# Optimization experiments

Measured on AMD Instinct MI355X. Metric: run time of the kernel, lower is better.

## Reference

```python
import jax, jax.numpy as jnp
import numpy as np


def setup_inputs() -> dict:
    key = jax.random.key(0)
    ks = jax.random.split(key, 32)
    B, S, H, E, Vs, T = 32, 400, 512, 300, 200, 32
    EN, V = 50000, 50200
    rn = lambda k, shape, s=0.05: jax.random.normal(k, shape, jnp.float32) * s
    return {
        'encoder_hidden': rn(ks[0], (B, S, 2 * H), 1.0),
        'hidden0': rn(ks[1], (B, H), 1.0),
        'user_embed': rn(ks[2], (B, E), 1.0),
        'W_embed': rn(ks[3], (EN, E), 1.0),
        'W_ih': rn(ks[4], (3 * H, E)), 'W_hh': rn(ks[5], (3 * H, H)),
        'b_ih': rn(ks[6], (3 * H,)), 'b_hh': rn(ks[7], (3 * H,)),
        'Wk_c': rn(ks[8], (2 * H, H)), 'bk_c': rn(ks[9], (H,)),
        'Wq_c': rn(ks[10], (H, H)), 'bq_c': rn(ks[11], (H,)),
        'we_c': rn(ks[12], (H,)), 'be_c': rn(ks[13], (1,)),
        'Wk_u': rn(ks[14], (E, H)), 'bk_u': rn(ks[15], (H,)),
        'Wq_u': rn(ks[16], (H, H)), 'bq_u': rn(ks[17], (H,)),
        'we_u': rn(ks[18], (H,)), 'be_u': rn(ks[19], (1,)),
        'Wc': rn(ks[20], (3 * H + 2 * E, H)),
        'Wg': rn(ks[21], (3 * H + E,)), 'bg': rn(ks[22], (1,)),
        'Wgen': rn(ks[23], (H, EN)),
        'src_mask': jnp.ones((B, S), jnp.int32),
        'tgt_': jax.random.randint(ks[24], (B, T), 0, EN),
        'specific_vocab': jax.random.randint(ks[25], (B, Vs), 0, EN),
        'vocab_size': V,
    }


def reference(encoder_hidden, hidden0, user_embed, W_embed, W_ih, W_hh, b_ih, b_hh,
              Wk_c, bk_c, Wq_c, bq_c, we_c, be_c, Wk_u, bk_u, Wq_u, bq_u, we_u, be_u,
              Wc, Wg, bg, Wgen, src_mask, tgt_, specific_vocab, vocab_size):
    B, T = tgt_.shape
    # teacher forcing: prev token embed, step 0 uses <s> token id 1
    tgt_embed = W_embed[tgt_]                                  # [B,T,E]
    init_embed = jnp.broadcast_to(W_embed[1], (B, 1, W_embed.shape[1]))
    prev = jnp.concatenate([init_embed, tgt_embed[:, :T - 1]], axis=1)
    xs = jnp.swapaxes(prev, 0, 1)                              # [T,B,E]

    user_vocab_emb = W_embed[specific_vocab]                   # [B,Vs,E]
    proj_key_c = encoder_hidden @ Wk_c + bk_c                  # [B,S,H]
    proj_key_u = user_vocab_emb @ Wk_u + bk_u                  # [B,Vs,H]
    mask = src_mask != 0
    batch_idx = jnp.arange(B)[:, None]

    def gru_cell(h, x):
        gi = x @ W_ih.T + b_ih
        gh = h @ W_hh.T + b_hh
        i_r, i_z, i_n = jnp.split(gi, 3, axis=-1)
        h_r, h_z, h_n = jnp.split(gh, 3, axis=-1)
        r = jax.nn.sigmoid(i_r + h_r)
        z = jax.nn.sigmoid(i_z + h_z)
        n = jnp.tanh(i_n + r * h_n)
        return (1.0 - z) * n + z * h

    def step(h, x):
        h = gru_cell(h, x)                                     # [B,H]
        q = h
        # Bahdanau attention over encoder states
        sc = jnp.tanh((q @ Wq_c + bq_c)[:, None, :] + proj_key_c) @ we_c + be_c  # [B,S]
        sc = jnp.where(mask, sc, -1e9)
        ac = jax.nn.softmax(sc, axis=-1)
        ctx_c = jnp.einsum('bs,bsd->bd', ac, encoder_hidden)   # [B,2H]
        # Bahdanau attention over user-specific vocab embeddings
        su = jnp.tanh((q @ Wq_u + bq_u)[:, None, :] + proj_key_u) @ we_u + be_u  # [B,Vs]
        au = jax.nn.softmax(su, axis=-1)
        ctx_u = jnp.einsum('bv,bve->be', au, user_vocab_emb)   # [B,E]
        ch = jnp.tanh(jnp.concatenate([q, ctx_c, ctx_u, user_embed], axis=-1) @ Wc)
        gen_prob = jax.nn.softmax(ch @ Wgen, axis=-1)          # [B,embed_num]
        gen_prob = jnp.pad(gen_prob, ((0, 0), (0, vocab_size - gen_prob.shape[-1])))
        copy_prob = jnp.zeros((B, vocab_size), gen_prob.dtype).at[batch_idx, specific_vocab].add(au)
        copy_p = jax.nn.sigmoid(jnp.concatenate([ctx_c, q, ctx_u], axis=-1) @ Wg + bg[0])[:, None]
        mix = copy_p * copy_prob + (1.0 - copy_p) * gen_prob   # [B,vocab]
        return h, mix

    _, probs = jax.lax.scan(step, hidden0, xs)                 # [T,B,V]
    return jnp.swapaxes(probs, 0, 1)                           # [B,T,V]
```

## Files before the change

kernel.cpp:

```cpp
#include <hip/hip_runtime.h>


typedef __attribute__((ext_vector_type(8))) short short8;
typedef __attribute__((ext_vector_type(4))) float f32x4;
typedef unsigned short us;

#define SCW (-2.8853900817779268f)

__device__ __forceinline__ float bf2f(us u) {
  return __uint_as_float(((unsigned)u) << 16);
}
__device__ __forceinline__ us f2bf(float f) {
  unsigned x = __float_as_uint(f);
  unsigned r = x + 0x7fffu + ((x >> 16) & 1u);
  return (us)(r >> 16);
}
__device__ __forceinline__ float fsigmoid(float x) { return 1.f / (1.f + __expf(-x)); }
__device__ __forceinline__ float ftanh(float x) {
  float t = __expf(-2.f * fabsf(x));
  float r = (1.f - t) / (1.f + t);
  return x >= 0.f ? r : -r;
}
__device__ __forceinline__ float ftanh_fast(float x) {
  float u = exp2f(SCW * fabsf(x));
  float r = (1.f - u) * __builtin_amdgcn_rcpf(1.f + u);
  return copysignf(r, x);
}

struct PP {
  const float *enc, *hidden0, *Wk_c, *Wk_u, *Wq_c, *Wq_u, *Wc, *W_ih, *W_hh, *W_embed;
  const int *tgt, *sv;
  us *encb, *hball, *WkcT, *WkuT, *WqcuT, *WcT, *WihT, *WhhF, *xe, *uve;
};

__device__ void tcast_job(const float* __restrict__ src, us* __restrict__ dst,
                          int R, int C, int Rpad, int x, int y, float scale,
                          int lt, float* tb) {
  int tx = lt & 31, ty = lt >> 5;
  int c0 = x * 32, r0 = y * 32;
#pragma unroll
  for (int i = 0; i < 4; ++i) {
// ... 252 lines not shown
#pragma unroll
    for (int q = 0; q < 2; ++q)
#pragma unroll
      for (int reg = 0; reg < 4; ++reg) {
        int r = m0 + m * 16 + (lane >> 4) * 4 + reg;
        int c = n0 + (w * 2 + q) * 16 + (lane & 15);
        float v = acc[m][q][reg];
        if (MODE == 0) v += bscale * bias[c];
        else v = ftanh_fast(v);
        outB[(size_t)r * N + c] = f2bf(v);
      }
}

struct FP {
  const us* frag; const us* gib; const float* bhh; const float* hidden0;
  us* hball; float* hfall; int* arrive;
  const us* xe; const us* WihT; const float* bih; us* gibout;
  const us* encb; const us* WkcT; const float* bkc; us* pkc;
  const us* uve; const us* WkuT; const float* bku; us* pku;
  const float* Wgen; us* WT;
  const float* enc; us* encTp;
  us* uveTp;
};

__device__ void gru_body(const FP& P, int q, int tid, char* pool) {
  us* hs = (us*)pool;
  float* gh = (float*)(pool + 32768);
  const int lane = tid & 63, w = tid >> 6;
  short8 bfr[16];
  {
    const us* fb = P.frag + (((size_t)(q * 12 + w) * 16) * 64 + lane) * 8;
#pragma unroll
    for (int kt = 0; kt < 16; ++kt) bfr[kt] = *(const short8*)(fb + (size_t)kt * 512);
  }
  float hprev[3];
#pragma unroll
  for (int s = 0; s < 3; ++s) {
    int i = tid + s * 768;
    if (i < 2048) {
      int b = i >> 6, jj = i & 63;
      hprev[s] = P.hidden0[b * 512 + q * 64 + jj];
    }
  }
  if (tid == 0) {
    while (__hip_atomic_load(P.arrive + 32, __ATOMIC_ACQUIRE,
                             __HIP_MEMORY_SCOPE_AGENT) < 48) {
      __builtin_amdgcn_s_sleep(1);
    }
  }
  __syncthreads();
  const int sw = (lane & 7) << 3;
  for (int t = 0; t < 32; ++t) {
    if (t > 0) {
      if (tid == 0) {
        while (__hip_atomic_load(P.arrive + (t - 1), __ATOMIC_ACQUIRE,
                                 __HIP_MEMORY_SCOPE_AGENT) < 8) {
          __builtin_amdgcn_s_sleep(1);
        }
      }
      __syncthreads();
    }
    const us* hp = P.hball + (size_t)t * 16384;
    for (int i = tid; i < 2048; i += 768)
      ((uint4*)hs)[i ^ ((i >> 6) & 7)] = *(const uint4*)(hp + i * 8);
    __syncthreads();
    f32x4 acc0 = {}, acc1 = {};
#pragma unroll
// ... 3 lines not shown
      short8 a0 = *(const short8*)(hs + base0);
      short8 a1 = *(const short8*)(hs + base1);
      acc0 = __builtin_amdgcn_mfma_f32_16x16x32_bf16(a0, bfr[kt], acc0, 0, 0, 0);
      acc1 = __builtin_amdgcn_mfma_f32_16x16x32_bf16(a1, bfr[kt], acc1, 0, 0, 0);
    }
    {
      int col = w * 16 + (lane & 15);
#pragma unroll
      for (int reg = 0; reg < 4; ++reg) {
        gh[col * 33 + ((lane >> 4) * 4 + reg)] = acc0[reg];
        gh[col * 33 + (16 + (lane >> 4) * 4 + reg)] = acc1[reg];
      }
    }
    __syncthreads();
    us* hbn = P.hball + (size_t)(t + 1) * 16384;
    float* hfn = P.hfall + (size_t)t * 16384;
#pragma unroll
    for (int s = 0; s < 3; ++s) {
      int i = tid + s * 768;
      if (i < 2048) {
        int b = i >> 6, jj = i & 63, j = q * 64 + jj;
        float g0 = gh[jj * 33 + b] + P.bhh[j];
        float g1 = gh[(64 + jj) * 33 + b] + P.bhh[512 + j];
        float g2 = gh[(128 + jj) * 33 + b] + P.bhh[1024 + j];
        size_t gbase = (size_t)(t * 32 + b) * 1536;
        float r_ = fsigmoid(bf2f(P.gib[gbase + j]) + g0);
        float z_ = fsigmoid(bf2f(P.gib[gbase + 512 + j]) + g1);
        float n_ = ftanh(bf2f(P.gib[gbase + 1024 + j]) + r_ * g2);
        float hv = (1.f - z_) * n_ + z_ * hprev[s];
        hprev[s] = hv;
        hbn[b * 512 + j] = f2bf(hv);
        hfn[b * 512 + j] = hv;
      }
    }
    __syncthreads();
    if (tid == 0)
      __hip_atomic_fetch_add(P.arrive + t, 1, __ATOMIC_RELEASE,
                             __HIP_MEMORY_SCOPE_AGENT);
  }
}

__device__ void gemm0_body(const us* A, const us* BT, int N, int K,
                           int mt, int nt, const float* bias, float bscale,
                           us* outB, int tid, char* pool) {
  us* As = (us*)pool;
  us* Bs = (us*)(pool + 16384);
  const bool act = tid < 512;
// ... 34 lines not shown
  }
  if (act) {
#pragma unroll
    for (int m = 0; m < 4; ++m)
#pragma unroll
      for (int n = 0; n < 4; ++n)
#pragma unroll
        for (int reg = 0; reg < 4; ++reg) {
          int r = m0 + wr * 64 + m * 16 + (lane >> 4) * 4 + reg;
          int c = n0 + wc * 64 + n * 16 + (lane & 15);
          outB[(size_t)r * N + c] = f2bf(acc[m][n][reg] + bscale * bias[c]);
        }
  }
}

__global__ __launch_bounds__(768, 1) void k_fat(FP P) {
  __shared__ char pool[98304];
  const int bid = blockIdx.x, tid = threadIdx.x;
  if (bid < 8) { gru_body(P, bid, tid, pool); return; }
  if (bid < 56) {
    int j = bid - 8;
    gemm0_body(P.xe, P.WihT, 1536, 320, j / 12, j % 12, P.bih, 1.f, P.gibout, tid, pool);
    __syncthreads();
    if (tid == 0)
      __hip_atomic_fetch_add(P.arrive + 32, 1, __ATOMIC_RELEASE,
                             __HIP_MEMORY_SCOPE_AGENT);
    return;
  }
  if (bid < 256) {
    int j = bid - 56;
    gemm0_body(P.encb, P.WkcT, 512, 1024, j >> 2, j & 3, P.bkc, SCW, P.pkc, tid, pool);
    return;
  }
  if (bid < 356) {
    int j = bid - 256;
    gemm0_body(P.uve, P.WkuT, 512, 320, j >> 2, j & 3, P.bku, SCW, P.pku, tid, pool);
    return;
  }
  const int g = tid >> 8, lt = tid & 255;
  const int tx = lt & 31, ty = lt >> 5;
  float* tb = (float*)(pool + g * 4224);
  if (bid < 878) {
    int base = (bid - 356) * 3 + g;
    for (int it = 0; it < 16; ++it) {
      int sub = base + it * 1566;
      bool valid = sub < 25008;
      int x = valid ? sub % 1563 : 0, y = valid ? sub / 1563 : 0;
      int c0 = x * 32, r0 = y * 32;
      if (valid) {
#pragma unroll
        for (int i = 0; i < 4; ++i) {
          int r = r0 + ty + i * 8, c = c0 + tx;
          tb[(ty + i * 8) * 33 + tx] =
              (c < 50000) ? P.Wgen[(size_t)r * 50000 + c] : 0.f;
        }
      }
      __syncthreads();
      if (valid) {
#pragma unroll
        for (int i = 0; i < 4; ++i) {
          int c = c0 + ty + i * 8;
          if (c < 50000)
            P.WT[(size_t)c * 512 + r0 + tx] = f2bf(tb[tx * 33 + ty + i * 8]);
        }
      }
      __syncthreads();
    }
    return;
  }
  if (bid < 1156) {
    int base = (bid - 878) * 3 + g;
    for (int it = 0; it < 16; ++it) {
      int sub = base + it * 834;
      bool valid = sub < 13312;
      int x = sub & 31, rem = sub >> 5;
      int y = rem % 13, z = rem / 13;
      const float* src = P.enc + (size_t)z * 409600;
      us* dst = P.encTp + (size_t)z * 425984;
      int c0 = x * 32, r0 = y * 32;
      if (valid) {
#pragma unroll
        for (int i = 0; i < 4; ++i) {
          int r = r0 + ty + i * 8, c = c0 + tx;
          tb[(ty + i * 8) * 33 + tx] = (r < 400) ? src[(size_t)r * 1024 + c] : 0.f;
        }
      }
      __syncthreads();
      if (valid) {
#pragma unroll
        for (int i = 0; i < 4; ++i) {
          int c = c0 + ty + i * 8, rr = r0 + tx;
          if (rr < 416) dst[(size_t)c * 416 + rr] = f2bf(tb[tx * 33 + ty + i * 8]);
        }
      }
      __syncthreads();
    }
    return;
  }
  {
    us* tbu = (us*)tb;
    int base = (bid - 1156) * 3 + g;
    for (int it = 0; it < 16; ++it) {
      int sub = base + it * 141;
      bool valid = sub < 2240;
      int x = sub % 10, rem = sub / 10;
      int y = rem % 7, z = rem / 7;
      const us* src = P.uve + (size_t)z * 64000;
      us* dst = P.uveTp + (size_t)z * 71680;
      int c0 = x * 32, r0 = y * 32;
      if (valid) {
#pragma unroll
        for (int i = 0; i < 4; ++i) {
          int r = r0 + ty + i * 8, c = c0 + tx;
          tbu[(ty + i * 8) * 33 + tx] = (r < 200) ? src[(size_t)r * 320 + c] : (us)0;
        }
      }
      __syncthreads();
      if (valid) {
#pragma unroll
        for (int i = 0; i < 4; ++i) {
          int c = c0 + ty + i * 8, rr = r0 + tx;
          if (rr < 224) dst[(size_t)c * 224 + rr] = tbu[tx * 33 + ty + i * 8];
        }
      }
      __syncthreads();
    }
  }
}

__global__ __launch_bounds__(256) void k_scores(const us* __restrict__ Qall,
                                                const us* __restrict__ pkc,
                                                const us* __restrict__ pku,
                                                const float* __restrict__ wec,
                                                const float* __restrict__ bec,
                                                const float* __restrict__ weu,
                                                const float* __restrict__ beu,
                                                const int* __restrict__ src_mask,
                                                float* __restrict__ sc_enc,
                                                float* __restrict__ sc_usr) {
  __shared__ us q[16 * 512];
  const int bid = blockIdx.x;
  const bool enc = bid < 1600;
  int b, s0, th, qoff, S;
  if (enc) {
    b = bid / 50;
    int r = bid % 50;
    s0 = (r >> 1) * 16; th = r & 1; qoff = 0; S = 400;
  } else {
    int j = bid - 1600;
    b = j / 26;
    int r = j % 26;
    s0 = (r >> 1) * 16; th = r & 1; qoff = 512; S = 200;
  }
  for (int i = threadIdx.x; i < 1024; i += 256) {
    int tt = th * 16 + (i >> 6), c8 = (i & 63) * 8;
    ((uint4*)q)[i] = *(const uint4*)(Qall + (size_t)(tt * 32 + b) * 1024 + qoff + c8);
  }
  const int w = threadIdx.x >> 6, lane = threadIdx.x & 63;
  const int d0 = lane * 8;
  const float* we = enc ? wec : weu;
  float wef[8];
  {
    float4 w0 = *(const float4*)(we + d0);
    float4 w1 = *(const float4*)(we + d0 + 4);
    wef[0] = w0.x; wef[1] = w0.y; wef[2] = w0.z; wef[3] = w0.w;
    wef[4] = w1.x; wef[5] = w1.y; wef[6] = w1.z; wef[7] = w1.w;
  }
  const float bias = enc ? bec[0] : beu[0];
  float pkf[4][8];
  int ss[4], validv[4], maskedv[4];
#pragma unroll
  for (int si = 0; si < 4; ++si) {
    int s = s0 + w * 4 + si;
    validv[si] = (s < S);
    int sc = validv[si] ? s : (S - 1);
    ss[si] = sc;
    const us* pk = enc ? pkc + ((size_t)b * 400 + sc) * 512
                       : pku + ((size_t)b * 200 + sc) * 512;
    uint4 pkv = *(const uint4*)(pk + d0);
    pkf[si][0] = bf2f((us)(pkv.x & 0xffff)); pkf[si][1] = bf2f((us)(pkv.x >> 16));
    pkf[si][2] = bf2f((us)(pkv.y & 0xffff)); pkf[si][3] = bf2f((us)(pkv.y >> 16));
    pkf[si][4] = bf2f((us)(pkv.z & 0xffff)); pkf[si][5] = bf2f((us)(pkv.z >> 16));
    pkf[si][6] = bf2f((us)(pkv.w & 0xffff)); pkf[si][7] = bf2f((us)(pkv.w >> 16));
    maskedv[si] = enc ? (src_mask[b * 400 + sc] == 0) : 0;
  }
  __syncthreads();
  for (int tl = 0; tl < 16; ++tl) {
    short8 qv = *(const short8*)(q + tl * 512 + d0);
    float qf[8];
#pragma unroll
    for (int d = 0; d < 8; ++d) qf[d] = bf2f((us)qv[d]);
#pragma unroll
    for (int si = 0; si < 4; ++si) {
      float a = 0.f;
#pragma unroll
      for (int d = 0; d < 8; ++d) {
        float x = qf[d] + pkf[si][d];
        float u = exp2f(-fabsf(x));
        float r2v = (1.f - u) * __builtin_amdgcn_rcpf(1.f + u);
        a = fmaf(copysignf(r2v, -x), wef[d], a);
      }
#pragma unroll
      for (int m = 1; m < 64; m <<= 1) a += __shfl_xor(a, m, 64);
      if (lane == 0 && validv[si]) {
        int t = th * 16 + tl;
        float v = a + bias;
        if (enc) sc_enc[(size_t)(t * 32 + b) * 400 + ss[si]] = maskedv[si] ? -1e9f : v;
        else sc_usr[(size_t)(t * 32 + b) * 200 + ss[si]] = v;
      }
    }
  }
}

__device__ __forceinline__ float bmax256(float v, float* r4, int tid) {
#pragma unroll
  for (int m = 1; m < 64; m <<= 1) v = fmaxf(v, __shfl_xor(v, m, 64));
  if ((tid & 63) == 0) r4[tid >> 6] = v;
  __syncthreads();
  float x = fmaxf(fmaxf(r4[0], r4[1]), fmaxf(r4[2], r4[3]));
  __syncthreads();
  return x;
}
__device__ __forceinline__ float bsum256(float v, float* r4, int tid) {
#pragma unroll
  for (int m = 1; m < 64; m <<= 1) v += __shfl_xor(v, m, 64);
  if ((tid & 63) == 0) r4[tid >> 6] = v;
  __syncthreads();
  float x = r4[0] + r4[1] + r4[2] + r4[3];
  __syncthreads();
  return x;
}

__global__ __launch_bounds__(256) void k_softmax(const float* __restrict__ sc_enc,
                                                 const float* __restrict__ sc_usr,
                                                 const float* __restrict__ bg,
                                                 us* __restrict__ AC,
                                                 us* __restrict__ AU,
                                                 float* __restrict__ aual,
                                                 float* __restrict__ cp_acc) {
  __shared__ float r4[4];
  int r = blockIdx.x, tid = threadIdx.x;
  if (r < 1024) {
    int t = r >> 5, b = r & 31;
    float v0 = (tid < 400) ? sc_enc[(size_t)r * 400 + tid] : -3e38f;
    float v1 = (tid + 256 < 400) ? sc_enc[(size_t)r * 400 + tid + 256] : -3e38f;
    float mx = bmax256(fmaxf(v0, v1), r4, tid);
    float e0 = (tid < 400) ? __expf(v0 - mx) : 0.f;
    float e1 = (tid + 256 < 400) ? __expf(v1 - mx) : 0.f;
    float inv = 1.f / bsum256(e0 + e1, r4, tid);
    us* ACb = AC + (size_t)(b * 32 + t) * 416;
    if (tid < 400) ACb[tid] = f2bf(e0 * inv);
    int s2 = tid + 256;
    if (s2 < 400) ACb[s2] = f2bf(e1 * inv);
    else if (s2 < 416) ACb[s2] = 0;
    if (tid == 0) cp_acc[r] = bg[0];
  } else {
    int rr = r - 1024;
    int t = rr >> 5, b = rr & 31;
    float v0 = (tid < 200) ? sc_usr[(size_t)rr * 200 + tid] : -3e38f;
    float mx = bmax256(v0, r4, tid);
    float e0 = (tid < 200) ? __expf(v0 - mx) : 0.f;
    float inv = 1.f / bsum256(e0, r4, tid);
    us* AUb = AU + (size_t)(b * 32 + t) * 224;
    if (tid < 200) {
      float a = e0 * inv;
      AUb[tid] = f2bf(a);
      aual[(size_t)rr * 200 + tid] = a;
    } else if (tid < 224) {
      AUb[tid] = 0;
    }
  }
}

__global__ __launch_bounds__(256) void k_ctx(const us* __restrict__ A,
                                             const us* __restrict__ BT,
                                             const float* __restrict__ Wg,
                                             us* __restrict__ catall,
                                             float* __restrict__ cp_acc,
                                             int N, int Kp, int catOff, int wgOff,
                                             int Nvalid) {
  __shared__ us As[32 * 32];
  __shared__ us Bs[128 * 32];
  __shared__ float gaccs[32];
  const int b = blockIdx.y, n0 = blockIdx.x * 128;
  const us* Ab = A + (size_t)b * 32 * Kp;
  const us* Bb = BT + (size_t)b * N * Kp;
  const int tid = threadIdx.x, lane = tid & 63, w = tid >> 6;
  if (tid < 32) gaccs[tid] = 0.f;
  f32x4 acc[2][2] = {};
  for (int kk = 0; kk < Kp; kk += 32) {
    uint4 av, bv0, bv1;
    if (tid < 128) av = *(const uint4*)(Ab + (size_t)(tid >> 2) * Kp + kk + (tid & 3) * 8);
    {
      int i0 = tid * 2, row0 = i0 >> 2, c0 = (i0 & 3) * 8;
      int i1 = tid * 2 + 1, row1 = i1 >> 2, c1 = (i1 & 3) * 8;
      int nr0 = n0 + row0; if (nr0 > N - 1) nr0 = N - 1;
      int nr1 = n0 + row1; if (nr1 > N - 1) nr1 = N - 1;
      bv0 = *(const uint4*)(Bb + (size_t)nr0 * Kp + kk + c0);
      bv1 = *(const uint4*)(Bb + (size_t)nr1 * Kp + kk + c1);
    }
    __syncthreads();
    if (tid < 128) ((uint4*)As)[tid] = av;
// ... 15 lines not shown
    for (int qq = 0; qq < 2; ++qq)
#pragma unroll
      for (int reg = 0; reg < 4; ++reg) {
        int t_ = mt * 16 + (lane >> 4) * 4 + reg;
        int c = n0 + (w * 2 + qq) * 16 + (lane & 15);
        if (c < Nvalid) {
          float v = acc[mt][qq][reg];
          catall[(size_t)(t_ * 32 + b) * 2144 + catOff + c] = f2bf(v);
          atomicAdd(&gaccs[t_], v * Wg[wgOff + c]);
        }
      }
  __syncthreads();
  if (tid < 32) atomicAdd(&cp_acc[tid * 32 + b], gaccs[tid]);
}

__global__ __launch_bounds__(256) void k_catgate(const us* __restrict__ hball,
                                                 const float* __restrict__ hfall,
                                                 const float* __restrict__ ue,
                                                 const float* __restrict__ Wg,
                                                 const float* __restrict__ cp_acc,
                                                 us* __restrict__ catall,
                                                 float* __restrict__ cp_all) {
  __shared__ float r4[4];
  int r = blockIdx.x, tid = threadIdx.x;
  int t = r >> 5, b = r & 31;
  us* row = catall + (size_t)r * 2144;
  const us* hb = hball + (size_t)(t + 1) * 16384 + b * 512;
  row[tid] = hb[tid];
  row[256 + tid] = hb[256 + tid];
  float gp = 0.f;
  for (int i = tid; i < 512; i += 256)
    gp += hfall[(size_t)t * 16384 + b * 512 + i] * Wg[1024 + i];
  for (int i = tid; i < 308; i += 256)
    row[1836 + i] = (i < 300) ? f2bf(ue[b * 300 + i]) : (us)0;
  float gtot = bsum256(gp, r4, tid);
  if (tid == 0) cp_all[r] = fsigmoid(gtot + cp_acc[r]);
}

__global__ __launch_bounds__(256) void k_finalize(float* __restrict__ out,
                                                  const float* __restrict__ rowsum,
                                                  const float* __restrict__ cp_all,
                                                  const float* __restrict__ au_all,
                                                  const int* __restrict__ sv) {
  int r = blockIdx.x;
  int t = threadIdx.x;
  int b = r & 31, tt = r >> 5;
  float cp = cp_all[r];
  float scale = (1.f - cp) / rowsum[r];
  float* base = out + (size_t)(b * 32 + tt) * 50200;
  float4* b4 = (float4*)base;
  for (int i = t; i < 12550; i += 256) {
    if (i < 12500) {
      float4 v = b4[i];
      v.x *= scale; v.y *= scale; v.z *= scale; v.w *= scale;
      b4[i] = v;
    } else {
      b4[i] = make_float4(0.f, 0.f, 0.f, 0.f);
    }
  }
  __syncthreads();
  if (t < 200) {
    int idx = sv[b * 200 + t];
    atomicAdd(base + idx, cp * au_all[(size_t)r * 200 + t]);
  }
}

__global__ __launch_bounds__(256) void k_finalize2(const us* __restrict__ expb,
                                                   const float* __restrict__ rowsum,
                                                   const float* __restrict__ cp_all,
                                                   const float* __restrict__ au_all,
                                                   const int* __restrict__ sv,
                                                   float* __restrict__ out) {
  int r = blockIdx.x;
  int t = threadIdx.x;
  int b = r & 31, tt = r >> 5;
  float cp = cp_all[r];
  float scale = (1.f - cp) / rowsum[r];
  size_t obase = (size_t)(b * 32 + tt) * 50200;
  const uint4* eb = (const uint4*)(expb + obase);
  float4* ob = (float4*)(out + obase);
  for (int i = t; i < 6275; i += 256) {
    float4 o0, o1;
    if (i < 6250) {
      uint4 ev = eb[i];
      o0.x = bf2f((us)(ev.x & 0xffff)) * scale; o0.y = bf2f((us)(ev.x >> 16)) * scale;
      o0.z = bf2f((us)(ev.y & 0xffff)) * scale; o0.w = bf2f((us)(ev.y >> 16)) * scale;
      o1.x = bf2f((us)(ev.z & 0xffff)) * scale; o1.y = bf2f((us)(ev.z >> 16)) * scale;
      o1.z = bf2f((us)(ev.w & 0xffff)) * scale; o1.w = bf2f((us)(ev.w >> 16)) * scale;
    } else {
      o0 = make_float4(0.f, 0.f, 0.f, 0.f);
      o1 = o0;
// ... 48 lines not shown
    char* p = base + off;
    off += (bytes + 255) & ~(size_t)255;
    return p;
  };
  us* WT = (us*)take(50000ull * 512 * 2);
  char* R0 = take(32ull * 1024 * 416 * 2);
  us* encb = (us*)R0;
  char* RCD = take(12800ull * 512 * 2 + 6400ull * 512 * 2);
  us* pkc = (us*)RCD;
  us* pku = (us*)(RCD + 12800ull * 512 * 2);
  us* AC = (us*)RCD;
  us* AU = (us*)(RCD + 860160);
  float* aual = (float*)(RCD + 860160 + 458752);
  us* catall = (us*)(RCD + 860160 + 458752 + 819200);
  us* chb = (us*)(RCD + 860160 + 458752 + 819200 + 4390912);
  char* RU = take(6400ull * 320 * 2);
  us* uve = (us*)RU;
  float* sc_enc = (float*)RU;
  float* sc_usr = (float*)(RU + 1024ull * 400 * 4);
  us* uveTp = (us*)take(32ull * 320 * 224 * 2);
  char* RG = take(2700000);
  us* WkcT = (us*)RG;
  us* WihT = (us*)(RG + 1048576);
  us* xe = (us*)(RG + 1048576 + 983040);
  us* Qall = (us*)RG;
  us* WkuT = (us*)take(512ull * 320 * 2);
  us* WqcuT = (us*)take(1024ull * 512 * 2);
  us* WcT = (us*)take(512ull * 2144 * 2);
  us* WhhF = (us*)take(1536ull * 512 * 2);
  us* gib = (us*)take(1024ull * 1536 * 2);
  us* hball = (us*)take(33ull * 16384 * 2);
  float* hfall = (float*)take(32ull * 16384 * 4);
  float* bqcu = (float*)take(1024 * 4);
  float* cp_acc = (float*)take(1024 * 4);
  float* cp_all = (float*)take(1024 * 4);
  float* rsum = (float*)take(1024 * 4);
  int* arrive = (int*)take(33 * 4);
  size_t expb_bytes = 1024ull * 50200 * 2;
  bool big_ws = (ws_size >= off + expb_bytes + 256);
  us* expb = big_ws ? (us*)take(expb_bytes) : nullptr;
  us* encTp = big_ws ? expb : (us*)R0;

  hipMemcpyAsync(bqcu, bq_c, 512 * 4, hipMemcpyDeviceToDevice, stream);
  hipMemcpyAsync(bqcu + 512, bq_u, 512 * 4, hipMemcpyDeviceToDevice, stream);
  hipMemsetAsync(rsum, 0, 1024 * 4, stream);
  hipMemsetAsync(arrive, 0, 33 * 4, stream);

  PP pp;
  pp.enc = enc; pp.hidden0 = hidden0; pp.Wk_c = Wk_c; pp.Wk_u = Wk_u;
  pp.Wq_c = Wq_c; pp.Wq_u = Wq_u; pp.Wc = Wc; pp.W_ih = W_ih; pp.W_hh = W_hh;
  pp.W_embed = W_embed; pp.tgt = tgt; pp.sv = sv;
  pp.encb = encb; pp.hball = hball; pp.WkcT = WkcT; pp.WkuT = WkuT;
  pp.WqcuT = WqcuT; pp.WcT = WcT; pp.WihT = WihT; pp.WhhF = WhhF;
  pp.xe = xe; pp.uve = uve;
  k_prep<<<5920, 256, 0, stream>>>(pp);

  FP fp;
  fp.frag = WhhF; fp.gib = gib; fp.bhh = b_hh; fp.hidden0 = hidden0;
  fp.hball = hball; fp.hfall = hfall; fp.arrive = arrive;
  fp.xe = xe; fp.WihT = WihT; fp.bih = b_ih; fp.gibout = gib;
  fp.encb = encb; fp.WkcT = WkcT; fp.bkc = bk_c; fp.pkc = pkc;
  fp.uve = uve; fp.WkuT = WkuT; fp.bku = bk_u; fp.pku = pku;
  fp.Wgen = Wgen; fp.WT = WT; fp.enc = enc; fp.encTp = encTp; fp.uveTp = uveTp;

  if (big_ws) {
    k_fat<<<1203, 768, 0, stream>>>(fp);
  } else {
    k_tcastX<<<dim3(1563, 16, 1), 256, 0, stream>>>(Wgen, WT, 512, 50000, 512, 0, 0);
    gemm_bt<0><<<200, 512, 0, stream>>>(encb, WkcT, 12800, 512, 1024, 4, bk_c, SCW,
                                        pkc, nullptr, nullptr);
    gemm_bt<0><<<100, 512, 0, stream>>>(uve, WkuT, 6400, 512, 320, 4, bk_u, SCW,
                                        pku, nullptr, nullptr);
    k_tcastX<<<dim3(32, 13, 32), 256, 0, stream>>>(enc, encTp, 400, 1024, 416,
                                                   400ull * 1024, 1024ull * 416);
    k_tcastXb<<<dim3(10, 7, 32), 256, 0, stream>>>(uve, uveTp, 200, 320, 224,
                                                   200ull * 320, 320ull * 224);
    k_fat<<<56, 768, 0, stream>>>(fp);
  }

  gemm_med<0><<<128, 256, 0, stream>>>(hball + 16384, WqcuT, 1024, 1024, 512, 8,
                                       bqcu, SCW, Qall);
  k_scores<<<2432, 256, 0, stream>>>(Qall, pkc, pku, we_c, be_c, we_u, be_u,
                                     src_mask, sc_enc, sc_usr);
  k_softmax<<<2048, 256, 0, stream>>>(sc_enc, sc_usr, bg, AC, AU, aual, cp_acc);
  k_ctx<<<dim3(8, 32), 256, 0, stream>>>(AC, encTp, Wg, catall, cp_acc,
                                         1024, 416, 512, 0, 1024);
  k_ctx<<<dim3(3, 32), 256, 0, stream>>>(AU, uveTp, Wg, catall, cp_acc,
                                         320, 224, 1536, 1536, 300);
  k_catgate<<<1024, 256, 0, stream>>>(hball, hfall, user_embed, Wg, cp_acc,
                                      catall, cp_all);
  gemm_med<2><<<64, 256, 0, stream>>>(catall, WcT, 1024, 512, 2144, 4, nullptr,
                                      1.f, chb);
  if (big_ws) {
    gemm_bt<3><<<4 * 391, 512, 0, stream>>>(chb, WT, 1024, 50000, 512, 391, nullptr,
                                            1.f, expb, nullptr, rsum);
    k_finalize2<<<1024, 256, 0, stream>>>(expb, rsum, cp_all, aual, sv, out);
  } else {
    gemm_bt<1><<<4 * 391, 512, 0, stream>>>(chb, WT, 1024, 50000, 512, 391, nullptr,
                                            1.f, nullptr, out, rsum);
    k_finalize<<<1024, 256, 0, stream>>>(out, rsum, cp_all, aual, sv);
  }
}
```

Before: 689.5 us.

## Overlap per-step query projection and attention scores with GRU recurrence in fat kernel

The input-gate GEMM moves out of the persistent fused kernel into a separate launch that runs before it, so the GRU blocks no longer wait on it. The fused kernel gains per-timestep query-projection and score blocks that spin on flags to run as soon as each GRU step and the key projections finish. Softmax is merged with the concat/gate kernel and the two context kernels are merged into one. The float hidden-state copy and the cp_all buffer are dropped, and the gate sigmoid moves into finalize. The fused kernel grows to many more blocks that spin-wait, which risks occupancy contention with the serial GRU chain, and gate-input loads are hoisted ahead of the per-step wait.

```diff
diff --git a/kernel.cpp b/kernel.cpp
--- a/kernel.cpp
+++ b/kernel.cpp
@@ -25,6 +25,12 @@
   float u = exp2f(SCW * fabsf(x));
   float r = (1.f - u) * __builtin_amdgcn_rcpf(1.f + u);
   return copysignf(r, x);
+}
+__device__ __forceinline__ void unpack8(uint4 v, float* f) {
+  f[0] = bf2f((us)(v.x & 0xffff)); f[1] = bf2f((us)(v.x >> 16));
+  f[2] = bf2f((us)(v.y & 0xffff)); f[3] = bf2f((us)(v.y >> 16));
+  f[4] = bf2f((us)(v.z & 0xffff)); f[5] = bf2f((us)(v.z >> 16));
+  f[6] = bf2f((us)(v.w & 0xffff)); f[7] = bf2f((us)(v.w >> 16));
 }
 
 struct PP {
@@ -307,13 +313,17 @@
 
 struct FP {
   const us* frag; const us* gib; const float* bhh; const float* hidden0;
-  us* hball; float* hfall; int* arrive;
-  const us* xe; const us* WihT; const float* bih; us* gibout;
+  us* hball; int* arrive;
   const us* encb; const us* WkcT; const float* bkc; us* pkc;
   const us* uve; const us* WkuT; const float* bku; us* pku;
   const float* Wgen; us* WT;
   const float* enc; us* encTp;
   us* uveTp;
+  const us* WqcuT; const float* bqcu; us* Qall;
+  int* qdone; int* pkdone;
+  const float *wec, *bec, *weu, *beu;
+  const int* src_mask;
+  float *sc_enc, *sc_usr;
 };
 
 __device__ void gru_body(const FP& P, int q, int tid, char* pool) {
@@ -335,15 +345,20 @@
       hprev[s] = P.hidden0[b * 512 + q * 64 + jj];
     }
   }
-  if (tid == 0) {
-    while (__hip_atomic_load(P.arrive + 32, __ATOMIC_ACQUIRE,
-                             __HIP_MEMORY_SCOPE_AGENT) < 48) {
-      __builtin_amdgcn_s_sleep(1);
-    }
-  }
-  __syncthreads();
   const int sw = (lane & 7) << 3;
   for (int t = 0; t < 32; ++t) {
+    float gi0[3], gi1[3], gi2[3];
+#pragma unroll
+    for (int s = 0; s < 3; ++s) {
+      int i = tid + s * 768;
+      if (i < 2048) {
+        int b = i >> 6, jj = i & 63, j = q * 64 + jj;
+        size_t gbase = (size_t)(t * 32 + b) * 1536;
+        gi0[s] = bf2f(P.gib[gbase + j]);
+        gi1[s] = bf2f(P.gib[gbase + 512 + j]);
+        gi2[s] = bf2f(P.gib[gbase + 1024 + j]);
+      }
+    }
     if (t > 0) {
       if (tid == 0) {
         while (__hip_atomic_load(P.arrive + (t - 1), __ATOMIC_ACQUIRE,
@@ -377,7 +392,6 @@
     }
     __syncthreads();
     us* hbn = P.hball + (size_t)(t + 1) * 16384;
-    float* hfn = P.hfall + (size_t)t * 16384;
 #pragma unroll
     for (int s = 0; s < 3; ++s) {
       int i = tid + s * 768;
@@ -386,14 +400,12 @@
         float g0 = gh[jj * 33 + b] + P.bhh[j];
         float g1 = gh[(64 + jj) * 33 + b] + P.bhh[512 + j];
         float g2 = gh[(128 + jj) * 33 + b] + P.bhh[1024 + j];
-        size_t gbase = (size_t)(t * 32 + b) * 1536;
-        float r_ = fsigmoid(bf2f(P.gib[gbase + j]) + g0);
-        float z_ = fsigmoid(bf2f(P.gib[gbase + 512 + j]) + g1);
-        float n_ = ftanh(bf2f(P.gib[gbase + 1024 + j]) + r_ * g2);
+        float r_ = fsigmoid(gi0[s] + g0);
+        float z_ = fsigmoid(gi1[s] + g1);
+        float n_ = ftanh(gi2[s] + r_ * g2);
         float hv = (1.f - z_) * n_ + z_ * hprev[s];
         hprev[s] = hv;
         hbn[b * 512 + j] = f2bf(hv);
-        hfn[b * 512 + j] = hv;
       }
     }
     __syncthreads();
@@ -458,34 +470,167 @@
   }
 }
 
+__device__ void q_body(const FP& P, int t, int nt, int tid, char* pool, bool doWait) {
+  us* As = (us*)pool;
+  us* Bs = (us*)(pool + 2048);
+  if (doWait) {
+    if (tid == 0) {
+      while (__hip_atomic_load(P.arrive + t, __ATOMIC_ACQUIRE,
+                               __HIP_MEMORY_SCOPE_AGENT) < 8) {
+        __builtin_amdgcn_s_sleep(1);
+      }
+    }
+    __syncthreads();
+  }
+  const bool act = tid < 256;
+  const us* A = P.hball + (size_t)(t + 1) * 16384;
+  const int lane = tid & 63, w = (tid >> 6) & 3;
+  const int n0 = nt * 128;
+  f32x4 acc[2][2] = {};
+  for (int kk = 0; kk < 512; kk += 32) {
+    uint4 av = {0, 0, 0, 0}, bv0 = {0, 0, 0, 0}, bv1 = {0, 0, 0, 0};
+    if (act) {
+      if (tid < 128) av = *(const uint4*)(A + (size_t)(tid >> 2) * 512 + kk + (tid & 3) * 8);
+      int i0 = tid * 2, i1 = tid * 2 + 1;
+      bv0 = *(const uint4*)(P.WqcuT + (size_t)(n0 + (i0 >> 2)) * 512 + kk + (i0 & 3) * 8);
+      bv1 = *(const uint4*)(P.WqcuT + (size_t)(n0 + (i1 >> 2)) * 512 + kk + (i1 & 3) * 8);
+    }
+    __syncthreads();
+    if (act) {
+      if (tid < 128) ((uint4*)As)[tid] = av;
+      ((uint4*)Bs)[tid * 2] = bv0;
+      ((uint4*)Bs)[tid * 2 + 1] = bv1;
+    }
+    __syncthreads();
+    if (act) {
+      short8 a0 = *(const short8*)(As + ((lane & 15)) * 32 + (lane >> 4) * 8);
+      short8 a1 = *(const short8*)(As + (16 + (lane & 15)) * 32 + (lane >> 4) * 8);
+#pragma unroll
+      for (int qq = 0; qq < 2; ++qq) {
+        short8 bf_ = *(const short8*)(Bs + ((w * 2 + qq) * 16 + (lane & 15)) * 32 + (lane >> 4) * 8);
+        acc[0][qq] = __builtin_amdgcn_mfma_f32_16x16x32_bf16(a0, bf_, acc[0][qq], 0, 0, 0);
+        acc[1][qq] = __builtin_amdgcn_mfma_f32_16x16x32_bf16(a1, bf_, acc[1][qq], 0, 0, 0);
+      }
+    }
+  }
+  if (act) {
+#pragma unroll
+    for (int mt = 0; mt < 2; ++mt)
+#pragma unroll
+      for (int qq = 0; qq < 2; ++qq)
+#pragma unroll
+        for (int reg = 0; reg < 4; ++reg) {
+          int b = mt * 16 + (lane >> 4) * 4 + reg;
+          int c = n0 + (w * 2 + qq) * 16 + (lane & 15);
+          P.Qall[(size_t)(t * 32 + b) * 1024 + c] =
+              f2bf(acc[mt][qq][reg] + SCW * P.bqcu[c]);
+        }
+  }
+  __syncthreads();
+  if (doWait && tid == 0)
+    __hip_atomic_fetch_add(P.qdone + t, 1, __ATOMIC_RELEASE,
+                           __HIP_MEMORY_SCOPE_AGENT);
+}
+
+__device__ void sc_body(const FP& P, int b, int t, int tid, int nthreads,
+                        bool doWait) {
+  if (doWait) {
+    if (tid == 0) {
+      while (__hip_atomic_load(P.pkdone, __ATOMIC_ACQUIRE,
+                               __HIP_MEMORY_SCOPE_AGENT) < 300) {
+        __builtin_amdgcn_s_sleep(1);
+      }
+      while (__hip_atomic_load(P.qdone + t, __ATOMIC_ACQUIRE,
+                               __HIP_MEMORY_SCOPE_AGENT) < 8) {
+        __builtin_amdgcn_s_sleep(1);
+      }
+    }
+    __syncthreads();
+  }
+  const int nw = nthreads >> 6;
+  const int w = tid >> 6, lane = tid & 63, d0 = lane * 8;
+  const int row = t * 32 + b;
+  float qe[8], qu[8], wee[8], weuu[8];
+  unpack8(*(const uint4*)(P.Qall + (size_t)row * 1024 + d0), qe);
+  unpack8(*(const uint4*)(P.Qall + (size_t)row * 1024 + 512 + d0), qu);
+  {
+    float4 a0 = *(const float4*)(P.wec + d0), a1 = *(const float4*)(P.wec + d0 + 4);
+    wee[0] = a0.x; wee[1] = a0.y; wee[2] = a0.z; wee[3] = a0.w;
+    wee[4] = a1.x; wee[5] = a1.y; wee[6] = a1.z; wee[7] = a1.w;
+    float4 b0 = *(const float4*)(P.weu + d0), b1 = *(const float4*)(P.weu + d0 + 4);
+    weuu[0] = b0.x; weuu[1] = b0.y; weuu[2] = b0.z; weuu[3] = b0.w;
+    weuu[4] = b1.x; weuu[5] = b1.y; weuu[6] = b1.z; weuu[7] = b1.w;
+  }
+  const float bece = P.bec[0], beuu2 = P.beu[0];
+  for (int s = w; s < 400; s += nw) {
+    float pkf[8];
+    unpack8(*(const uint4*)(P.pkc + ((size_t)(b * 400 + s)) * 512 + d0), pkf);
+    float a = 0.f;
+#pragma unroll
+    for (int d = 0; d < 8; ++d) {
+      float x = qe[d] + pkf[d];
+      float u = exp2f(-fabsf(x));
+      float r2 = (1.f - u) * __builtin_amdgcn_rcpf(1.f + u);
+      a = fmaf(copysignf(r2, -x), wee[d], a);
+    }
+#pragma unroll
+    for (int m = 1; m < 64; m <<= 1) a += __shfl_xor(a, m, 64);
+    if (lane == 0)
+      P.sc_enc[(size_t)row * 400 + s] =
+          (P.src_mask[b * 400 + s] == 0) ? -1e9f : a + bece;
+  }
+  for (int s = w; s < 200; s += nw) {
+    float pkf[8];
+    unpack8(*(const uint4*)(P.pku + ((size_t)(b * 200 + s)) * 512 + d0), pkf);
+    float a = 0.f;
+#pragma unroll
+    for (int d = 0; d < 8; ++d) {
+      float x = qu[d] + pkf[d];
+      float u = exp2f(-fabsf(x));
+      float r2 = (1.f - u) * __builtin_amdgcn_rcpf(1.f + u);
+      a = fmaf(copysignf(r2, -x), weuu[d], a);
+    }
+#pragma unroll
+    for (int m = 1; m < 64; m <<= 1) a += __shfl_xor(a, m, 64);
+    if (lane == 0) P.sc_usr[(size_t)row * 200 + s] = a + beuu2;
+  }
+}
+
 __global__ __launch_bounds__(768, 1) void k_fat(FP P) {
-  __shared__ char pool[98304];
+  __shared__ char pool[58368];
   const int bid = blockIdx.x, tid = threadIdx.x;
   if (bid < 8) { gru_body(P, bid, tid, pool); return; }
-  if (bid < 56) {
+  if (bid < 208) {
     int j = bid - 8;
-    gemm0_body(P.xe, P.WihT, 1536, 320, j / 12, j % 12, P.bih, 1.f, P.gibout, tid, pool);
+    gemm0_body(P.encb, P.WkcT, 512, 1024, j >> 2, j & 3, P.bkc, SCW, P.pkc, tid, pool);
     __syncthreads();
     if (tid == 0)
-      __hip_atomic_fetch_add(P.arrive + 32, 1, __ATOMIC_RELEASE,
-                             __HIP_MEMORY_SCOPE_AGENT);
+      __hip_atomic_fetch_add(P.pkdone, 1, __ATOMIC_RELEASE, __HIP_MEMORY_SCOPE_AGENT);
     return;
   }
-  if (bid < 256) {
-    int j = bid - 56;
-    gemm0_body(P.encb, P.WkcT, 512, 1024, j >> 2, j & 3, P.bkc, SCW, P.pkc, tid, pool);
+  if (bid < 308) {
+    int j = bid - 208;
+    gemm0_body(P.uve, P.WkuT, 512, 320, j >> 2, j & 3, P.bku, SCW, P.pku, tid, pool);
+    __syncthreads();
+    if (tid == 0)
+      __hip_atomic_fetch_add(P.pkdone, 1, __ATOMIC_RELEASE, __HIP_MEMORY_SCOPE_AGENT);
     return;
   }
-  if (bid < 356) {
-    int j = bid - 256;
-    gemm0_body(P.uve, P.WkuT, 512, 320, j >> 2, j & 3, P.bku, SCW, P.pku, tid, pool);
+  if (bid >= 1155 && bid < 1411) {
+    int j = bid - 1155;
+    q_body(P, j >> 3, j & 7, tid, pool, true);
+    return;
+  }
+  if (bid >= 1411) {
+    int j = bid - 1411;
+    sc_body(P, j & 31, j >> 5, tid, 768, true);
     return;
   }
   const int g = tid >> 8, lt = tid & 255;
   const int tx = lt & 31, ty = lt >> 5;
   float* tb = (float*)(pool + g * 4224);
-  if (bid < 878) {
-    int base = (bid - 356) * 3 + g;
+  if (bid < 830) {
+    int base = (bid - 308) * 3 + g;
     for (int it = 0; it < 16; ++it) {
       int sub = base + it * 1566;
       bool valid = sub < 25008;
@@ -512,8 +657,8 @@
     }
     return;
   }
-  if (bid < 1156) {
-    int base = (bid - 878) * 3 + g;
+  if (bid < 1108) {
+    int base = (bid - 830) * 3 + g;
     for (int it = 0; it < 16; ++it) {
       int sub = base + it * 834;
       bool valid = sub < 13312;
@@ -543,7 +688,7 @@
   }
   {
     us* tbu = (us*)tb;
-    int base = (bid - 1156) * 3 + g;
+    int base = (bid - 1108) * 3 + g;
     for (int it = 0; it < 16; ++it) {
       int sub = base + it * 141;
       bool valid = sub < 2240;
@@ -572,88 +717,14 @@
   }
 }
 
-__global__ __launch_bounds__(256) void k_scores(const us* __restrict__ Qall,
-                                                const us* __restrict__ pkc,
-                                                const us* __restrict__ pku,
-                                                const float* __restrict__ wec,
-                                                const float* __restrict__ bec,
-                                                const float* __restrict__ weu,
-                                                const float* __restrict__ beu,
-                                                const int* __restrict__ src_mask,
-                                                float* __restrict__ sc_enc,
-                                                float* __restrict__ sc_usr) {
-  __shared__ us q[16 * 512];
-  const int bid = blockIdx.x;
-  const bool enc = bid < 1600;
-  int b, s0, th, qoff, S;
-  if (enc) {
-    b = bid / 50;
-    int r = bid % 50;
-    s0 = (r >> 1) * 16; th = r & 1; qoff = 0; S = 400;
-  } else {
-    int j = bid - 1600;
-    b = j / 26;
-    int r = j % 26;
-    s0 = (r >> 1) * 16; th = r & 1; qoff = 512; S = 200;
-  }
-  for (int i = threadIdx.x; i < 1024; i += 256) {
-    int tt = th * 16 + (i >> 6), c8 = (i & 63) * 8;
-    ((uint4*)q)[i] = *(const uint4*)(Qall + (size_t)(tt * 32 + b) * 1024 + qoff + c8);
-  }
-  const int w = threadIdx.x >> 6, lane = threadIdx.x & 63;
-  const int d0 = lane * 8;
-  const float* we = enc ? wec : weu;
-  float wef[8];
-  {
-    float4 w0 = *(const float4*)(we + d0);
-    float4 w1 = *(const float4*)(we + d0 + 4);
-    wef[0] = w0.x; wef[1] = w0.y; wef[2] = w0.z; wef[3] = w0.w;
-    wef[4] = w1.x; wef[5] = w1.y; wef[6] = w1.z; wef[7] = w1.w;
-  }
-  const float bias = enc ? bec[0] : beu[0];
-  float pkf[4][8];
-  int ss[4], validv[4], maskedv[4];
-#pragma unroll
-  for (int si = 0; si < 4; ++si) {
-    int s = s0 + w * 4 + si;
-    validv[si] = (s < S);
-    int sc = validv[si] ? s : (S - 1);
-    ss[si] = sc;
-    const us* pk = enc ? pkc + ((size_t)b * 400 + sc) * 512
-                       : pku + ((size_t)b * 200 + sc) * 512;
-    uint4 pkv = *(const uint4*)(pk + d0);
-    pkf[si][0] = bf2f((us)(pkv.x & 0xffff)); pkf[si][1] = bf2f((us)(pkv.x >> 16));
-    pkf[si][2] = bf2f((us)(pkv.y & 0xffff)); pkf[si][3] = bf2f((us)(pkv.y >> 16));
-    pkf[si][4] = bf2f((us)(pkv.z & 0xffff)); pkf[si][5] = bf2f((us)(pkv.z >> 16));
-    pkf[si][6] = bf2f((us)(pkv.w & 0xffff)); pkf[si][7] = bf2f((us)(pkv.w >> 16));
-    maskedv[si] = enc ? (src_mask[b * 400 + sc] == 0) : 0;
-  }
-  __syncthreads();
-  for (int tl = 0; tl < 16; ++tl) {
-    short8 qv = *(const short8*)(q + tl * 512 + d0);
-    float qf[8];
-#pragma unroll
-    for (int d = 0; d < 8; ++d) qf[d] = bf2f((us)qv[d]);
-#pragma unroll
-    for (int si = 0; si < 4; ++si) {
-      float a = 0.f;
-#pragma unroll
-      for (int d = 0; d < 8; ++d) {
-        float x = qf[d] + pkf[si][d];
-        float u = exp2f(-fabsf(x));
-        float r2v = (1.f - u) * __builtin_amdgcn_rcpf(1.f + u);
-        a = fmaf(copysignf(r2v, -x), wef[d], a);
-      }
-#pragma unroll
-      for (int m = 1; m < 64; m <<= 1) a += __shfl_xor(a, m, 64);
-      if (lane == 0 && validv[si]) {
-        int t = th * 16 + tl;
-        float v = a + bias;
-        if (enc) sc_enc[(size_t)(t * 32 + b) * 400 + ss[si]] = maskedv[si] ? -1e9f : v;
-        else sc_usr[(size_t)(t * 32 + b) * 200 + ss[si]] = v;
-      }
-    }
-  }
+__global__ __launch_bounds__(256) void k_qjob(FP P) {
+  __shared__ char pool[10240];
+  int j = blockIdx.x;
+  q_body(P, j >> 3, j & 7, threadIdx.x, pool, false);
+}
+__global__ __launch_bounds__(256) void k_scjob(FP P) {
+  int j = blockIdx.x;
+  sc_body(P, j & 31, j >> 5, threadIdx.x, 256, false);
 }
 
 __device__ __forceinline__ float bmax256(float v, float* r4, int tid) {
@@ -675,19 +746,22 @@
   return x;
 }
 
-__global__ __launch_bounds__(256) void k_softmax(const float* __restrict__ sc_enc,
-                                                 const float* __restrict__ sc_usr,
-                                                 const float* __restrict__ bg,
-                                                 us* __restrict__ AC,
-                                                 us* __restrict__ AU,
-                                                 float* __restrict__ aual,
-                                                 float* __restrict__ cp_acc) {
+__global__ __launch_bounds__(256) void k_soft2(const float* __restrict__ sc_enc,
+                                               const float* __restrict__ sc_usr,
+                                               us* __restrict__ AC,
+                                               us* __restrict__ AU,
+                                               float* __restrict__ aual,
+                                               float* __restrict__ cp_acc,
+                                               const us* __restrict__ hball,
+                                               const float* __restrict__ ue,
+                                               const float* __restrict__ Wg,
+                                               us* __restrict__ catall) {
   __shared__ float r4[4];
-  int r = blockIdx.x, tid = threadIdx.x;
-  if (r < 1024) {
-    int t = r >> 5, b = r & 31;
-    float v0 = (tid < 400) ? sc_enc[(size_t)r * 400 + tid] : -3e38f;
-    float v1 = (tid + 256 < 400) ? sc_enc[(size_t)r * 400 + tid + 256] : -3e38f;
+  int bid = blockIdx.x, tid = threadIdx.x;
+  if (bid < 1024) {
+    int t = bid >> 5, b = bid & 31;
+    float v0 = (tid < 400) ? sc_enc[(size_t)bid * 400 + tid] : -3e38f;
+    float v1 = (tid + 256 < 400) ? sc_enc[(size_t)bid * 400 + tid + 256] : -3e38f;
     float mx = bmax256(fmaxf(v0, v1), r4, tid);
     float e0 = (tid < 400) ? __expf(v0 - mx) : 0.f;
     float e1 = (tid + 256 < 400) ? __expf(v1 - mx) : 0.f;
@@ -697,9 +771,8 @@
     int s2 = tid + 256;
     if (s2 < 400) ACb[s2] = f2bf(e1 * inv);
     else if (s2 < 416) ACb[s2] = 0;
-    if (tid == 0) cp_acc[r] = bg[0];
-  } else {
-    int rr = r - 1024;
+  } else if (bid < 2048) {
+    int rr = bid - 1024;
     int t = rr >> 5, b = rr & 31;
     float v0 = (tid < 200) ? sc_usr[(size_t)rr * 200 + tid] : -3e38f;
     float mx = bmax256(v0, r4, tid);
@@ -713,23 +786,39 @@
     } else if (tid < 224) {
       AUb[tid] = 0;
     }
-  }
-}
-
-__global__ __launch_bounds__(256) void k_ctx(const us* __restrict__ A,
-                                             const us* __restrict__ BT,
-                                             const float* __restrict__ Wg,
-                                             us* __restrict__ catall,
-                                             float* __restrict__ cp_acc,
-                                             int N, int Kp, int catOff, int wgOff,
-                                             int Nvalid) {
-  __shared__ us As[32 * 32];
-  __shared__ us Bs[128 * 32];
-  __shared__ float gaccs[32];
-  const int b = blockIdx.y, n0 = blockIdx.x * 128;
-  const us* Ab = A + (size_t)b * 32 * Kp;
-  const us* Bb = BT + (size_t)b * N * Kp;
-  const int tid = threadIdx.x, lane = tid & 63, w = tid >> 6;
+  } else if (bid < 2304) {
+    int w = tid >> 6, lane = tid & 63;
+    int row = (bid - 2048) * 4 + w;
+    int t = row >> 5, b = row & 31;
+    us* rowp = catall + (size_t)row * 2144;
+    const us* hb = hball + (size_t)(t + 1) * 16384 + b * 512;
+    *(uint4*)(rowp + lane * 8) = *(const uint4*)(hb + lane * 8);
+    for (int i = lane; i < 308; i += 64)
+      rowp[1836 + i] = (i < 300) ? f2bf(ue[b * 300 + i]) : (us)0;
+  } else {
+    int w = tid >> 6, lane = tid & 63, d0 = lane * 8;
+#pragma unroll
+    for (int k = 0; k < 2; ++k) {
+      int row = (bid - 2304) * 8 + w * 2 + k;
+      int t = row >> 5, b = row & 31;
+      float hv[8];
+      unpack8(*(const uint4*)(hball + (size_t)(t + 1) * 16384 + b * 512 + d0), hv);
+      float4 g0 = *(const float4*)(Wg + 1024 + d0);
+      float4 g1 = *(const float4*)(Wg + 1024 + d0 + 4);
+      float a = hv[0] * g0.x + hv[1] * g0.y + hv[2] * g0.z + hv[3] * g0.w +
+                hv[4] * g1.x + hv[5] * g1.y + hv[6] * g1.z + hv[7] * g1.w;
+#pragma unroll
+      for (int m = 1; m < 64; m <<= 1) a += __shfl_xor(a, m, 64);
+      if (lane == 0) atomicAdd(&cp_acc[row], a);
+    }
+  }
+}
+
+__device__ void ctx_core(const us* Ab, const us* Bb, const float* Wg,
+                         us* catall, float* cp_acc, int b, int N, int Kp,
+                         int n0, int catOff, int wgOff, int Nvalid, int tid,
+                         us* As, us* Bs, float* gaccs) {
+  const int lane = tid & 63, w = tid >> 6;
   if (tid < 32) gaccs[tid] = 0.f;
   f32x4 acc[2][2] = {};
   for (int kk = 0; kk < Kp; kk += 32) {
@@ -775,38 +864,38 @@
   if (tid < 32) atomicAdd(&cp_acc[tid * 32 + b], gaccs[tid]);
 }
 
-__global__ __launch_bounds__(256) void k_catgate(const us* __restrict__ hball,
-                                                 const float* __restrict__ hfall,
-                                                 const float* __restrict__ ue,
-                                                 const float* __restrict__ Wg,
-                                                 const float* __restrict__ cp_acc,
-                                                 us* __restrict__ catall,
-                                                 float* __restrict__ cp_all) {
-  __shared__ float r4[4];
-  int r = blockIdx.x, tid = threadIdx.x;
-  int t = r >> 5, b = r & 31;
-  us* row = catall + (size_t)r * 2144;
-  const us* hb = hball + (size_t)(t + 1) * 16384 + b * 512;
-  row[tid] = hb[tid];
-  row[256 + tid] = hb[256 + tid];
-  float gp = 0.f;
-  for (int i = tid; i < 512; i += 256)
-    gp += hfall[(size_t)t * 16384 + b * 512 + i] * Wg[1024 + i];
-  for (int i = tid; i < 308; i += 256)
-    row[1836 + i] = (i < 300) ? f2bf(ue[b * 300 + i]) : (us)0;
-  float gtot = bsum256(gp, r4, tid);
-  if (tid == 0) cp_all[r] = fsigmoid(gtot + cp_acc[r]);
+__global__ __launch_bounds__(256) void k_ctx2(const us* __restrict__ AC,
+                                              const us* __restrict__ encTp,
+                                              const us* __restrict__ AU,
+                                              const us* __restrict__ uveTp,
+                                              const float* __restrict__ Wg,
+                                              us* __restrict__ catall,
+                                              float* __restrict__ cp_acc) {
+  __shared__ us As[32 * 32];
+  __shared__ us Bs[128 * 32];
+  __shared__ float gaccs[32];
+  int bid = blockIdx.x, tid = threadIdx.x;
+  if (bid < 256) {
+    int b = bid >> 3, nt = bid & 7;
+    ctx_core(AC + (size_t)b * 32 * 416, encTp + (size_t)b * 1024 * 416, Wg,
+             catall, cp_acc, b, 1024, 416, nt * 128, 512, 0, 1024, tid, As, Bs, gaccs);
+  } else {
+    int j = bid - 256;
+    int b = j / 3, nt = j % 3;
+    ctx_core(AU + (size_t)b * 32 * 224, uveTp + (size_t)b * 320 * 224, Wg,
+             catall, cp_acc, b, 320, 224, nt * 128, 1536, 1536, 300, tid, As, Bs, gaccs);
+  }
 }
 
 __global__ __launch_bounds__(256) void k_finalize(float* __restrict__ out,
                                                   const float* __restrict__ rowsum,
-                                                  const float* __restrict__ cp_all,
+                                                  const float* __restrict__ cp_acc,
+                                                  const float* __restrict__ bg,
                                                   const float* __restrict__ au_all,
                                                   const int* __restrict__ sv) {
-  int r = blockIdx.x;
-  int t = threadIdx.x;
+  int r = blockIdx.x, t = threadIdx.x;
   int b = r & 31, tt = r >> 5;
-  float cp = cp_all[r];
+  float cp = fsigmoid(cp_acc[r] + bg[0]);
   float scale = (1.f - cp) / rowsum[r];
   float* base = out + (size_t)(b * 32 + tt) * 50200;
   float4* b4 = (float4*)base;
@@ -828,14 +917,14 @@
 
 __global__ __launch_bounds__(256) void k_finalize2(const us* __restrict__ expb,
                                                    const float* __restrict__ rowsum,
-                                                   const float* __restrict__ cp_all,
+                                                   const float* __restrict__ cp_acc,
+                                                   const float* __restrict__ bg,
                                                    const float* __restrict__ au_all,
                                                    const int* __restrict__ sv,
                                                    float* __restrict__ out) {
-  int r = blockIdx.x;
-  int t = threadIdx.x;
+  int r = blockIdx.x, t = threadIdx.x;
   int b = r & 31, tt = r >> 5;
-  float cp = cp_all[r];
+  float cp = fsigmoid(cp_acc[r] + bg[0]);
   float scale = (1.f - cp) / rowsum[r];
   size_t obase = (size_t)(b * 32 + tt) * 50200;
   const uint4* eb = (const uint4*)(expb + obase);
@@ -914,28 +1003,28 @@
   float* aual = (float*)(RCD + 860160 + 458752);
   us* catall = (us*)(RCD + 860160 + 458752 + 819200);
   us* chb = (us*)(RCD + 860160 + 458752 + 819200 + 4390912);
-  char* RU = take(6400ull * 320 * 2);
-  us* uve = (us*)RU;
-  float* sc_enc = (float*)RU;
-  float* sc_usr = (float*)(RU + 1024ull * 400 * 4);
+  us* uve = (us*)take(6400ull * 320 * 2);
   us* uveTp = (us*)take(32ull * 320 * 224 * 2);
   char* RG = take(2700000);
   us* WkcT = (us*)RG;
   us* WihT = (us*)(RG + 1048576);
   us* xe = (us*)(RG + 1048576 + 983040);
-  us* Qall = (us*)RG;
   us* WkuT = (us*)take(512ull * 320 * 2);
   us* WqcuT = (us*)take(1024ull * 512 * 2);
   us* WcT = (us*)take(512ull * 2144 * 2);
   us* WhhF = (us*)take(1536ull * 512 * 2);
   us* gib = (us*)take(1024ull * 1536 * 2);
   us* hball = (us*)take(33ull * 16384 * 2);
-  float* hfall = (float*)take(32ull * 16384 * 4);
+  us* Qall = (us*)take(1024ull * 1024 * 2);
+  float* sc_enc = (float*)take(1024ull * 400 * 4);
+  float* sc_usr = (float*)take(1024ull * 200 * 4);
   float* bqcu = (float*)take(1024 * 4);
   float* cp_acc = (float*)take(1024 * 4);
-  float* cp_all = (float*)take(1024 * 4);
   float* rsum = (float*)take(1024 * 4);
-  int* arrive = (int*)take(33 * 4);
+  int* flags = (int*)take(65 * 4);
+  int* arrive = flags;
+  int* qdone = flags + 32;
+  int* pkdone = flags + 64;
   size_t expb_bytes = 1024ull * 50200 * 2;
   bool big_ws = (ws_size >= off + expb_bytes + 256);
   us* expb = big_ws ? (us*)take(expb_bytes) : nullptr;
@@ -944,7 +1033,8 @@
   hipMemcpyAsync(bqcu, bq_c, 512 * 4, hipMemcpyDeviceToDevice, stream);
   hipMemcpyAsync(bqcu + 512, bq_u, 512 * 4, hipMemcpyDeviceToDevice, stream);
   hipMemsetAsync(rsum, 0, 1024 * 4, stream);
-  hipMemsetAsync(arrive, 0, 33 * 4, stream);
+  hipMemsetAsync(cp_acc, 0, 1024 * 4, stream);
+  hipMemsetAsync(flags, 0, 65 * 4, stream);
 
   PP pp;
   pp.enc = enc; pp.hidden0 = hidden0; pp.Wk_c = Wk_c; pp.Wk_u = Wk_u;
@@ -954,17 +1044,21 @@
   pp.WqcuT = WqcuT; pp.WcT = WcT; pp.WihT = WihT; pp.WhhF = WhhF;
   pp.xe = xe; pp.uve = uve;
   k_prep<<<5920, 256, 0, stream>>>(pp);
+  gemm_med<0><<<192, 256, 0, stream>>>(xe, WihT, 1024, 1536, 320, 12, b_ih, 1.f, gib);
 
   FP fp;
   fp.frag = WhhF; fp.gib = gib; fp.bhh = b_hh; fp.hidden0 = hidden0;
-  fp.hball = hball; fp.hfall = hfall; fp.arrive = arrive;
-  fp.xe = xe; fp.WihT = WihT; fp.bih = b_ih; fp.gibout = gib;
+  fp.hball = hball; fp.arrive = arrive;
   fp.encb = encb; fp.WkcT = WkcT; fp.bkc = bk_c; fp.pkc = pkc;
   fp.uve = uve; fp.WkuT = WkuT; fp.bku = bk_u; fp.pku = pku;
   fp.Wgen = Wgen; fp.WT = WT; fp.enc = enc; fp.encTp = encTp; fp.uveTp = uveTp;
+  fp.WqcuT = WqcuT; fp.bqcu = bqcu; fp.Qall = Qall;
+  fp.qdone = qdone; fp.pkdone = pkdone;
+  fp.wec = we_c; fp.bec = be_c; fp.weu = we_u; fp.beu = be_u;
+  fp.src_mask = src_mask; fp.sc_enc = sc_enc; fp.sc_usr = sc_usr;
 
   if (big_ws) {
-    k_fat<<<1203, 768, 0, stream>>>(fp);
+    k_fat<<<2435, 768, 0, stream>>>(fp);
   } else {
     k_tcastX<<<dim3(1563, 16, 1), 256, 0, stream>>>(Wgen, WT, 512, 50000, 512, 0, 0);
     gemm_bt<0><<<200, 512, 0, stream>>>(encb, WkcT, 12800, 512, 1024, 4, bk_c, SCW,
@@ -975,29 +1069,23 @@
                                                    400ull * 1024, 1024ull * 416);
     k_tcastXb<<<dim3(10, 7, 32), 256, 0, stream>>>(uve, uveTp, 200, 320, 224,
                                                    200ull * 320, 320ull * 224);
-    k_fat<<<56, 768, 0, stream>>>(fp);
-  }
-
-  gemm_med<0><<<128, 256, 0, stream>>>(hball + 16384, WqcuT, 1024, 1024, 512, 8,
-                                       bqcu, SCW, Qall);
-  k_scores<<<2432, 256, 0, stream>>>(Qall, pkc, pku, we_c, be_c, we_u, be_u,
-                                     src_mask, sc_enc, sc_usr);
-  k_softmax<<<2048, 256, 0, stream>>>(sc_enc, sc_usr, bg, AC, AU, aual, cp_acc);
-  k_ctx<<<dim3(8, 32), 256, 0, stream>>>(AC, encTp, Wg, catall, cp_acc,
-                                         1024, 416, 512, 0, 1024);
-  k_ctx<<<dim3(3, 32), 256, 0, stream>>>(AU, uveTp, Wg, catall, cp_acc,
-                                         320, 224, 1536, 1536, 300);
-  k_catgate<<<1024, 256, 0, stream>>>(hball, hfall, user_embed, Wg, cp_acc,
-                                      catall, cp_all);
+    k_fat<<<8, 768, 0, stream>>>(fp);
+    k_qjob<<<256, 256, 0, stream>>>(fp);
+    k_scjob<<<1024, 256, 0, stream>>>(fp);
+  }
+
+  k_soft2<<<2432, 256, 0, stream>>>(sc_enc, sc_usr, AC, AU, aual, cp_acc,
+                                    hball, user_embed, Wg, catall);
+  k_ctx2<<<352, 256, 0, stream>>>(AC, encTp, AU, uveTp, Wg, catall, cp_acc);
   gemm_med<2><<<64, 256, 0, stream>>>(catall, WcT, 1024, 512, 2144, 4, nullptr,
                                       1.f, chb);
   if (big_ws) {
     gemm_bt<3><<<4 * 391, 512, 0, stream>>>(chb, WT, 1024, 50000, 512, 391, nullptr,
                                             1.f, expb, nullptr, rsum);
-    k_finalize2<<<1024, 256, 0, stream>>>(expb, rsum, cp_all, aual, sv, out);
+    k_finalize2<<<1024, 256, 0, stream>>>(expb, rsum, cp_acc, bg, aual, sv, out);
   } else {
     gemm_bt<1><<<4 * 391, 512, 0, stream>>>(chb, WT, 1024, 50000, 512, 391, nullptr,
                                             1.f, nullptr, out, rsum);
-    k_finalize<<<1024, 256, 0, stream>>>(out, rsum, cp_all, aual, sv);
-  }
-}
+    k_finalize<<<1024, 256, 0, stream>>>(out, rsum, cp_acc, bg, aual, sv);
+  }
+}
```

Measured after the change: 726.4 us. 1.05x slower.
